# Performance work log

Measured on AMD Instinct MI355X. Metric: run time of the kernel, lower is better.

Reference implementation:

```python
import jax, jax.numpy as jnp
import numpy as np

DILATED_K = 3  # init kwarg dilated_parameter_k -> 2**k = 8


def setup_inputs() -> dict:
    key = jax.random.key(0)
    k1, k2, k3, k4 = jax.random.split(key, 4)
    B, H, R, F = 16, 8, 400, 256
    A = jax.random.uniform(k1, (B, H, R, R), dtype=jnp.float32)
    feats = jax.random.normal(k2, (B, H, R, F), dtype=jnp.float32)
    # Linear(features, features) params (torch layout: weight [out, in], bias [out])
    lim = 1.0 / np.sqrt(F)
    W = jax.random.uniform(k3, (F, F), dtype=jnp.float32, minval=-lim, maxval=lim)
    b = jax.random.uniform(k4, (F,), dtype=jnp.float32, minval=-lim, maxval=lim)
    return {"Adjancy_Matrix": A, "features": feats, "W": W, "b": b}


def reference(Adjancy_Matrix, features, W, b):
    # Deterministic reference: takes the prob < 0.8 (dilated) branch of the
    # original module (the other branch is pure random dropout of the mask).
    two_k = 2 ** DILATED_K  # 8
    # torch.sort(A, descending=True, dim=3).indices == argsort of -A along last dim
    idx = jnp.argsort(-Adjancy_Matrix, axis=3)  # [B,H,R,R] int32
    # mask = 1 where sorted column index is 0 or in {2^k, ..., 2^k+4}
    mask = (idx == 0) | ((idx >= two_k) & (idx <= two_k + 4))
    R = Adjancy_Matrix.shape[2]
    mask = mask | jnp.eye(R, dtype=bool)  # add identity per (b, h), clamp >=1 -> 1
    masked_A = Adjancy_Matrix * mask.astype(Adjancy_Matrix.dtype)
    agg = jnp.einsum('bhij,bhjf->bhif', masked_A, features)  # [B,H,R,F]
    out = jax.nn.relu(agg @ W.T + b)
    return out + features
```

## Files before the change

### kernel.cpp

```cpp
#include <hip/hip_runtime.h>

typedef unsigned short u16;
typedef unsigned int   u32;
typedef unsigned long long u64;
typedef __bf16 bf16x8 __attribute__((ext_vector_type(8)));
typedef float  f32x4  __attribute__((ext_vector_type(4)));
typedef u32    u32x4  __attribute__((ext_vector_type(4)));
typedef u16    u16x4  __attribute__((ext_vector_type(4)));
typedef u16    u16x8v __attribute__((ext_vector_type(8)));

#define R_DIM 400
#define F_DIM 256
#define M_TOT 51200

__device__ __forceinline__ u16 f2bf(float f) {
    union { float f; u32 i; } x; x.f = f;
    u32 r = x.i + 0x7FFFu + ((x.i >> 16) & 1u);
    return (u16)(r >> 16);
}

__global__ __launch_bounds__(256) void wprep_f32(const float* __restrict__ W,
                                                 u16* __restrict__ Wf) {
    int g  = blockIdx.x * 256 + threadIdx.x;
    int ks = g >> 10;
    int T  = (g >> 6) & 15;
    int L  = g & 63;
    int n  = T * 16 + (L & 15);
    int k  = ks * 32 + (L >> 4) * 8;
    const float* wp = W + (size_t)n * F_DIM + k;
    float4 lo = *(const float4*)wp;
    float4 hi = *(const float4*)(wp + 4);
    u16x8v t;
    t[0] = f2bf(lo.x); t[1] = f2bf(lo.y); t[2] = f2bf(lo.z); t[3] = f2bf(lo.w);
    t[4] = f2bf(hi.x); t[5] = f2bf(hi.y); t[6] = f2bf(hi.z); t[7] = f2bf(hi.w);
    *(u16x8v*)(Wf + (size_t)g * 8) = t;
}

__device__ __forceinline__ void compute_slots(float4 v0, float4 v1r, int lane,
                                              int diag, u32 es[7], u32* dup_out) {
    float4 v1 = v1r;
    if (lane >= 36) { v1.x = -1.f; v1.y = -1.f; v1.z = -1.f; v1.w = -1.f; }
    float refs[6];
    refs[0] = __shfl(v0.x, 0);
    refs[1] = __shfl(v0.x, 2);
    refs[2] = __shfl(v0.y, 2);
    refs[3] = __shfl(v0.z, 2);
    refs[4] = __shfl(v0.w, 2);
    refs[5] = __shfl(v0.x, 3);
    const int cols[6] = {0, 8, 9, 10, 11, 12};
    float e0[4] = {v0.x, v0.y, v0.z, v0.w};
    float e1[4] = {v1.x, v1.y, v1.z, v1.w};
    u32 cnt[6];
#pragma unroll
    for (int k = 0; k < 6; k++) {
        int c = 0;
#pragma unroll
        for (int jj = 0; jj < 4; jj++) {
            int j = (lane << 2) + jj;
            c += __popcll(__ballot(e0[jj] > refs[k] ||
                                   (e0[jj] == refs[k] && j < cols[k])));
            c += __popcll(__ballot(e1[jj] > refs[k]));
        }
        cnt[k] = (u32)c;
    }
    bool dup = (diag == (int)cnt[0]) | (diag == (int)cnt[1]) | (diag == (int)cnt[2]) |
               (diag == (int)cnt[3]) | (diag == (int)cnt[4]) | (diag == (int)cnt[5]);
#pragma unroll
    for (int s = 0; s < 6; s++) es[s] = cnt[s];
    es[6] = (u32)diag;
    *dup_out = dup ? 1u : 0u;
}

__global__ __launch_bounds__(64, 3) void gcn_fused(const float* __restrict__ A,
                                                   const float* __restrict__ feats,
                                                   const u16*  __restrict__ Wf,
                                                   const float* __restrict__ bias,
                                                   float* __restrict__ out) {
    __shared__ __align__(16) u16 agg_lds[16][264];
    __shared__ __align__(16) u16 probeA[16][32];
    __shared__ __align__(16) u16 probeB[16][32];

    const int lane = threadIdx.x & 63;
    const int bid = (int)blockIdx.x;
    const int m0  = ((bid & 7) * 400 + (bid >> 3)) * 16;
    const int kg  = (lane >> 4) << 3;
    const int bh  = m0 / R_DIM;
    const int i0  = m0 - bh * R_DIM;

    for (int e = lane; e < 512; e += 64) {
        int r = e >> 5, k = e & 31;
        probeA[r][k] = (k == 0) ? f2bf((float)r) : ((k == 1) ? f2bf(1.0f) : (u16)0);
        probeB[r][k] = (k == 0) ? f2bf(16.0f)    : ((k == 1) ? f2bf((float)r) : (u16)0);
    }

    const float* Ab = A + (size_t)m0 * R_DIM;
    const float* fb = feats + (size_t)bh * R_DIM * F_DIM + lane * 4;

    {
        float4 a0b[3], a1b[3];
        float  wb[3][7];
        float4 fbv[3][7];
        u32    dupb[3];

#pragma unroll
        for (int p = 0; p < 2; p++) {
            const float* Ar = Ab + (size_t)p * R_DIM;
            a0b[p] = *(const float4*)(Ar + lane * 4);
            a1b[p] = *(const float4*)(Ar + (lane < 36 ? 256 + lane * 4 : 0));
        }

#pragma unroll
        for (int rr = 0; rr < 16; rr++) {
            if (rr + 2 < 16) {
                const float* An = Ab + (size_t)(rr + 2) * R_DIM;
                a0b[(rr + 2) % 3] = *(const float4*)(An + lane * 4);
                a1b[(rr + 2) % 3] = *(const float4*)(An + (lane < 36 ? 256 + lane * 4 : 0));
            }

            u32 es[7], dupm;
            compute_slots(a0b[rr % 3], a1b[rr % 3], lane, i0 + rr, es, &dupm);
            dupb[rr % 3] = dupm;

            const float* Ar = Ab + (size_t)rr * R_DIM;
#pragma unroll
            for (int s = 0; s < 7; s++) {
                u32 e = es[s];
                wb[rr % 3][s]  = Ar[e];
                fbv[rr % 3][s] = *(const float4*)(fb + (size_t)e * F_DIM);
            }

            if (rr >= 2) {
                const int rc = rr - 2, bi = rc % 3;
                float a0 = 0.f, a1 = 0.f, a2 = 0.f, a3 = 0.f;
#pragma unroll
                for (int s = 0; s < 7; s++) {
                    float ws = (s == 6 && dupb[bi]) ? 0.f : wb[bi][s];
                    a0 += ws * fbv[bi][s].x; a1 += ws * fbv[bi][s].y;
                    a2 += ws * fbv[bi][s].z; a3 += ws * fbv[bi][s].w;
                }
                u16x4 st = { f2bf(a0), f2bf(a1), f2bf(a2), f2bf(a3) };
                *(u16x4*)&agg_lds[rc][lane * 4] = st;
            }
        }
#pragma unroll
        for (int rc = 14; rc < 16; rc++) {
            const int bi = rc % 3;
            float a0 = 0.f, a1 = 0.f, a2 = 0.f, a3 = 0.f;
#pragma unroll
            for (int s = 0; s < 7; s++) {
                float ws = (s == 6 && dupb[bi]) ? 0.f : wb[bi][s];
                a0 += ws * fbv[bi][s].x; a1 += ws * fbv[bi][s].y;
                a2 += ws * fbv[bi][s].z; a3 += ws * fbv[bi][s].w;
            }
            u16x4 st = { f2bf(a0), f2bf(a1), f2bf(a2), f2bf(a3) };
            *(u16x4*)&agg_lds[rc][lane * 4] = st;
        }
    }

    int rowi[4], coli[4];
    {
        bf16x8 pa = *(const bf16x8*)&probeA[lane & 15][kg];
        bf16x8 pb = *(const bf16x8*)&probeB[lane & 15][kg];
        f32x4 pd = {0.f, 0.f, 0.f, 0.f};
        pd = __builtin_amdgcn_mfma_f32_16x16x32_bf16(pa, pb, pd, 0, 0, 0);
#pragma unroll
        for (int reg = 0; reg < 4; reg++) {
            int v = (int)(pd[reg] + 0.5f);
            rowi[reg] = v >> 4;
            coli[reg] = v & 15;
        }
    }

    f32x4 acc[16];
#pragma unroll
    for (int nt = 0; nt < 16; nt++) acc[nt] = (f32x4){0.f, 0.f, 0.f, 0.f};

#pragma unroll
    for (int ks = 0; ks < 8; ks++) {
        bf16x8 af = *(const bf16x8*)&agg_lds[lane & 15][ks * 32 + kg];
#pragma unroll
        for (int nt = 0; nt < 16; nt++) {
            u32x4 v = *(const u32x4*)(Wf + ((size_t)(ks * 16 + nt) * 64 + lane) * 8);
            bf16x8 b = __builtin_bit_cast(bf16x8, v);
            acc[nt] = __builtin_amdgcn_mfma_f32_16x16x32_bf16(af, b, acc[nt], 0, 0, 0);
        }
    }

#pragma unroll
    for (int nt = 0; nt < 16; nt++) {
        int nb = nt * 16;
#pragma unroll
        for (int reg = 0; reg < 4; reg++) {
            int gn = nb + coli[reg];
            float bn = bias[gn];
            int gm = m0 + rowi[reg];
            size_t off = (size_t)gm * F_DIM + gn;
            out[off] = fmaxf(acc[nt][reg] + bn, 0.f) + feats[off];
        }
    }
}

extern "C" void kernel_launch(void* const* d_in, const int* in_sizes, int n_in,
                              void* d_out, int out_size, void* d_ws, size_t ws_size,
                              hipStream_t stream) {
    const float* A     = (const float*)d_in[0];
    const float* feats = (const float*)d_in[1];
    const float* W     = (const float*)d_in[2];
    const float* bias  = (const float*)d_in[3];
    float* out = (float*)d_out;

    u16* Wf = (u16*)d_ws;

    wprep_f32<<<32, 256, 0, stream>>>(W, Wf);
    gcn_fused<<<M_TOT / 16, 64, 0, stream>>>(A, feats, Wf, bias, out);
}
```

Measured before the change: 253.6 us.

## Split fused GCN kernel into separate gather and GEMM kernels via bf16 workspace

Replaces the single-wave fused kernel with two launches. A gather kernel uses one wave per row to compute the mask slots and write the aggregated row as bf16 to a global workspace. A 256-thread GEMM kernel then reads that workspace, with each wave covering a 16x128 output tile. This trades the software-pipelined per-row loop and LDS staging for more parallelism and occupancy, at the cost of an extra global round trip for the aggregate (about 26 MB) and an extra launch.

After: 211.7 us. 16.5% less time.

```diff
diff --git a/kernel.cpp b/kernel.cpp
--- a/kernel.cpp
+++ b/kernel.cpp
@@ -71,91 +71,61 @@
     *dup_out = dup ? 1u : 0u;
 }
 
-__global__ __launch_bounds__(64, 3) void gcn_fused(const float* __restrict__ A,
-                                                   const float* __restrict__ feats,
+__global__ __launch_bounds__(256, 4) void gcn_gather(const float* __restrict__ A,
+                                                     const float* __restrict__ feats,
+                                                     u16* __restrict__ agg) {
+    const int tid = threadIdx.x, wid = tid >> 6, lane = tid & 63;
+    const int bid = (int)blockIdx.x;
+    const int row = ((bid & 7) * 1600 + (bid >> 3)) * 4 + wid;
+    const int bh  = row / R_DIM;
+    const int dia = row - bh * R_DIM;
+
+    const float* Ar = A + (size_t)row * R_DIM;
+    float4 v0 = *(const float4*)(Ar + lane * 4);
+    float4 v1 = *(const float4*)(Ar + (lane < 36 ? 256 + lane * 4 : 0));
+
+    u32 es[7], dupm;
+    compute_slots(v0, v1, lane, dia, es, &dupm);
+
+    const float* fb = feats + (size_t)bh * R_DIM * F_DIM + lane * 4;
+    float w[7]; float4 f[7];
+#pragma unroll
+    for (int s = 0; s < 7; s++) {
+        u32 e = es[s];
+        w[s] = Ar[e];
+        f[s] = *(const float4*)(fb + (size_t)e * F_DIM);
+    }
+    float a0 = 0.f, a1 = 0.f, a2 = 0.f, a3 = 0.f;
+#pragma unroll
+    for (int s = 0; s < 7; s++) {
+        float ws = (s == 6 && dupm) ? 0.f : w[s];
+        a0 += ws * f[s].x; a1 += ws * f[s].y; a2 += ws * f[s].z; a3 += ws * f[s].w;
+    }
+    u16x4 st = { f2bf(a0), f2bf(a1), f2bf(a2), f2bf(a3) };
+    *(u16x4*)(agg + (size_t)row * F_DIM + lane * 4) = st;
+}
+
+__global__ __launch_bounds__(256, 4) void gcn_gemm(const u16*  __restrict__ agg,
                                                    const u16*  __restrict__ Wf,
                                                    const float* __restrict__ bias,
+                                                   const float* __restrict__ feats,
                                                    float* __restrict__ out) {
-    __shared__ __align__(16) u16 agg_lds[16][264];
     __shared__ __align__(16) u16 probeA[16][32];
     __shared__ __align__(16) u16 probeB[16][32];
 
-    const int lane = threadIdx.x & 63;
+    const int tid = threadIdx.x, wid = tid >> 6, lane = tid & 63;
     const int bid = (int)blockIdx.x;
-    const int m0  = ((bid & 7) * 400 + (bid >> 3)) * 16;
+    const int m0  = ((bid & 7) * 200 + (bid >> 3)) * 32;
     const int kg  = (lane >> 4) << 3;
-    const int bh  = m0 / R_DIM;
-    const int i0  = m0 - bh * R_DIM;
+    const int mt  = wid & 1;
+    const int nh  = wid >> 1;
 
-    for (int e = lane; e < 512; e += 64) {
+    for (int e = tid; e < 512; e += 256) {
         int r = e >> 5, k = e & 31;
         probeA[r][k] = (k == 0) ? f2bf((float)r) : ((k == 1) ? f2bf(1.0f) : (u16)0);
         probeB[r][k] = (k == 0) ? f2bf(16.0f)    : ((k == 1) ? f2bf((float)r) : (u16)0);
     }
-
-    const float* Ab = A + (size_t)m0 * R_DIM;
-    const float* fb = feats + (size_t)bh * R_DIM * F_DIM + lane * 4;
-
-    {
-        float4 a0b[3], a1b[3];
-        float  wb[3][7];
-        float4 fbv[3][7];
-        u32    dupb[3];
-
-#pragma unroll
-        for (int p = 0; p < 2; p++) {
-            const float* Ar = Ab + (size_t)p * R_DIM;
-            a0b[p] = *(const float4*)(Ar + lane * 4);
-            a1b[p] = *(const float4*)(Ar + (lane < 36 ? 256 + lane * 4 : 0));
-        }
-
-#pragma unroll
-        for (int rr = 0; rr < 16; rr++) {
-            if (rr + 2 < 16) {
-                const float* An = Ab + (size_t)(rr + 2) * R_DIM;
-                a0b[(rr + 2) % 3] = *(const float4*)(An + lane * 4);
-                a1b[(rr + 2) % 3] = *(const float4*)(An + (lane < 36 ? 256 + lane * 4 : 0));
-            }
-
-            u32 es[7], dupm;
-            compute_slots(a0b[rr % 3], a1b[rr % 3], lane, i0 + rr, es, &dupm);
-            dupb[rr % 3] = dupm;
-
-            const float* Ar = Ab + (size_t)rr * R_DIM;
-#pragma unroll
-            for (int s = 0; s < 7; s++) {
-                u32 e = es[s];
-                wb[rr % 3][s]  = Ar[e];
-                fbv[rr % 3][s] = *(const float4*)(fb + (size_t)e * F_DIM);
-            }
-
-            if (rr >= 2) {
-                const int rc = rr - 2, bi = rc % 3;
-                float a0 = 0.f, a1 = 0.f, a2 = 0.f, a3 = 0.f;
-#pragma unroll
-                for (int s = 0; s < 7; s++) {
-                    float ws = (s == 6 && dupb[bi]) ? 0.f : wb[bi][s];
-                    a0 += ws * fbv[bi][s].x; a1 += ws * fbv[bi][s].y;
-                    a2 += ws * fbv[bi][s].z; a3 += ws * fbv[bi][s].w;
-                }
-                u16x4 st = { f2bf(a0), f2bf(a1), f2bf(a2), f2bf(a3) };
-                *(u16x4*)&agg_lds[rc][lane * 4] = st;
-            }
-        }
-#pragma unroll
-        for (int rc = 14; rc < 16; rc++) {
-            const int bi = rc % 3;
-            float a0 = 0.f, a1 = 0.f, a2 = 0.f, a3 = 0.f;
-#pragma unroll
-            for (int s = 0; s < 7; s++) {
-                float ws = (s == 6 && dupb[bi]) ? 0.f : wb[bi][s];
-                a0 += ws * fbv[bi][s].x; a1 += ws * fbv[bi][s].y;
-                a2 += ws * fbv[bi][s].z; a3 += ws * fbv[bi][s].w;
-            }
-            u16x4 st = { f2bf(a0), f2bf(a1), f2bf(a2), f2bf(a3) };
-            *(u16x4*)&agg_lds[rc][lane * 4] = st;
-        }
-    }
+    __syncthreads();
 
     int rowi[4], coli[4];
     {
@@ -171,29 +141,31 @@
         }
     }
 
-    f32x4 acc[16];
+    f32x4 acc[8];
 #pragma unroll
-    for (int nt = 0; nt < 16; nt++) acc[nt] = (f32x4){0.f, 0.f, 0.f, 0.f};
+    for (int nt = 0; nt < 8; nt++) acc[nt] = (f32x4){0.f, 0.f, 0.f, 0.f};
 
+    const u16* ab = agg + (size_t)(m0 + mt * 16 + (lane & 15)) * F_DIM + kg;
 #pragma unroll
     for (int ks = 0; ks < 8; ks++) {
-        bf16x8 af = *(const bf16x8*)&agg_lds[lane & 15][ks * 32 + kg];
+        bf16x8 af = *(const bf16x8*)(ab + ks * 32);
 #pragma unroll
-        for (int nt = 0; nt < 16; nt++) {
-            u32x4 v = *(const u32x4*)(Wf + ((size_t)(ks * 16 + nt) * 64 + lane) * 8);
+        for (int nt = 0; nt < 8; nt++) {
+            int T = nh * 8 + nt;
+            u32x4 v = *(const u32x4*)(Wf + ((size_t)(ks * 16 + T) * 64 + lane) * 8);
             bf16x8 b = __builtin_bit_cast(bf16x8, v);
             acc[nt] = __builtin_amdgcn_mfma_f32_16x16x32_bf16(af, b, acc[nt], 0, 0, 0);
         }
     }
 
 #pragma unroll
-    for (int nt = 0; nt < 16; nt++) {
-        int nb = nt * 16;
+    for (int nt = 0; nt < 8; nt++) {
+        int nb = (nh * 8 + nt) * 16;
 #pragma unroll
         for (int reg = 0; reg < 4; reg++) {
             int gn = nb + coli[reg];
             float bn = bias[gn];
-            int gm = m0 + rowi[reg];
+            int gm = m0 + mt * 16 + rowi[reg];
             size_t off = (size_t)gm * F_DIM + gn;
             out[off] = fmaxf(acc[nt][reg] + bn, 0.f) + feats[off];
         }
@@ -209,8 +181,10 @@
     const float* bias  = (const float*)d_in[3];
     float* out = (float*)d_out;
 
-    u16* Wf = (u16*)d_ws;
+    u16* Wf  = (u16*)d_ws;
+    u16* agg = (u16*)((char*)d_ws + (size_t)128 * 1024);
 
-    wprep_f32<<<32, 256, 0, stream>>>(W, Wf);
-    gcn_fused<<<M_TOT / 16, 64, 0, stream>>>(A, feats, Wf, bias, out);
+    wprep_f32 <<<32,    256, 0, stream>>>(W, Wf);
+    gcn_gather<<<12800, 256, 0, stream>>>(A, feats, agg);
+    gcn_gemm  <<<1600,  256, 0, stream>>>(agg, Wf, bias, feats, out);
 }
```
